# Performance work log

Measured on AMD Instinct MI355X. Metric: run time of the kernel, lower is better.

The kernel has to match this reference:

```python
import jax, jax.numpy as jnp
import numpy as np


def _retain(o1, others, W, bias):
    # o1: (b, s, h); others: (b, 4, s, h); W: (h, h); bias: (1,)
    q = o1 @ W                                        # (b, s, h)
    scores = jnp.einsum('bih,bkjh->bijk', q, others) + bias[0]  # (b, s1, s2, 4)
    w = jax.nn.softmax(scores, axis=-1)               # softmax over the 4 options
    # weight[:, :, :, k] @ option_k summed over k
    return jnp.einsum('bijk,bkjh->bih', w, others)


def setup_inputs() -> dict:
    key = jax.random.key(0)
    ks = jax.random.split(key, 7)
    b, s, h = 32, 256, 1024
    opts = {f'option{i+1}': jax.random.normal(ks[i], (b, s, h), dtype=jnp.float32)
            for i in range(5)}
    W = 0.02 * jax.random.normal(ks[5], (h, h), dtype=jnp.float32)
    bias = 0.02 * jax.random.normal(ks[6], (1,), dtype=jnp.float32)
    return {**opts, 'W': W, 'bias': bias}


def reference(option1, option2, option3, option4, option5, W, bias):
    opts = [option1, option2, option3, option4, option5]
    total = None
    for i in range(5):
        others = jnp.stack([opts[j] for j in range(5) if j != i], axis=1)  # (b,4,s,h)
        r = _retain(opts[i], others, W, bias)
        total = r if total is None else total + r
    return total / 2.0
```

## Files before the change

### kernel.cpp

```cpp
#include <hip/hip_runtime.h>
#include <hip/hip_bf16.h>
#include <stdint.h>


#define BB 32
#define SS 256
#define HH 1024

typedef __attribute__((ext_vector_type(4))) float f32x4;
typedef __attribute__((ext_vector_type(8))) __bf16 bf16x8;
typedef __attribute__((ext_vector_type(4))) __bf16 bf16x4;

__device__ constexpr int PAIR(int i, int n) { return i * 4 + (n > i ? n - 1 : n); }

__device__ __forceinline__ void gload_lds16(const void* g, void* l) {
  __builtin_amdgcn_global_load_lds((const __attribute__((address_space(1))) void*)g,
                                   (__attribute__((address_space(3))) void*)l, 16, 0, 0);
}

__global__ void canary(float* out, float v) { out[0] = v; }

__global__ __launch_bounds__(256) void cast_all(
    const float* p0, const float* p1, const float* p2, const float* p3, const float* p4,
    __bf16* __restrict__ dst)
{
  int m = blockIdx.x >> 12;
  long off = ((long)(blockIdx.x & 4095) * 256 + threadIdx.x) * 8;
  const float* src = m == 0 ? p0 : m == 1 ? p1 : m == 2 ? p2 : m == 3 ? p3 : p4;
  float4 v0 = *(const float4*)(src + off);
  float4 v1 = *(const float4*)(src + off + 4);
  bf16x8 h;
  h[0] = (__bf16)v0.x; h[1] = (__bf16)v0.y; h[2] = (__bf16)v0.z; h[3] = (__bf16)v0.w;
  h[4] = (__bf16)v1.x; h[5] = (__bf16)v1.y; h[6] = (__bf16)v1.z; h[7] = (__bf16)v1.w;
  *(bf16x8*)(dst + (long)m * BB * SS * HH + off) = h;
}

__global__ __launch_bounds__(256) void cast_trW(const float* __restrict__ src,
                                                __bf16* __restrict__ dstT)
{
  __shared__ __bf16 tile[64][72];
  int ct = blockIdx.x & 15, rt = blockIdx.x >> 4;
  const float* s = src + (long)(rt * 64) * 1024 + ct * 64;
  int t = threadIdx.x;
#pragma unroll
  for (int p = 0; p < 4; p++) {
    int c = t + p * 256;
    int row = c >> 4, c4 = c & 15;
    float4 v = *(const float4*)(s + (long)row * 1024 + c4 * 4);
    bf16x4 h;
    h[0] = (__bf16)v.x; h[1] = (__bf16)v.y; h[2] = (__bf16)v.z; h[3] = (__bf16)v.w;
    *(bf16x4*)&tile[row][c4 * 4] = h;
  }
  __syncthreads();
#pragma unroll
  for (int p = 0; p < 4; p++) {
    int c = t + p * 256;
    int hr = c >> 4, s4 = c & 15;
    bf16x4 h;
    h[0] = tile[s4 * 4 + 0][hr];
    h[1] = tile[s4 * 4 + 1][hr];
    h[2] = tile[s4 * 4 + 2][hr];
    h[3] = tile[s4 * 4 + 3][hr];
    *(bf16x4*)(dstT + (long)(ct * 64 + hr) * 1024 + rt * 64 + s4 * 4) = h;
  }
}

__global__ __launch_bounds__(256, 3) void qgemm_b16(
    const __bf16* __restrict__ A, const __bf16* __restrict__ Bt, __bf16* __restrict__ C)
{
  __shared__ __align__(16) char ldsb[3 * 16384];
  int lin = blockIdx.x;
  int xcd = lin & 7, idx = lin >> 3;
  int rt = xcd * 40 + (idx >> 3), ct = idx & 7;
  int t = threadIdx.x, l = t & 63, w = t >> 6;
  int wm = w >> 1, wn = w & 1;
  f32x4 acc[4][4] = {};

  const char *gA0, *gA1, *gB0, *gB1;
  {
    int c0 = t, c1 = t + 256;
    int r0 = c0 >> 2, h0 = (c0 & 3) ^ ((c0 >> 3) & 3);
    int r1 = c1 >> 2, h1 = (c1 & 3) ^ ((c1 >> 3) & 3);
    gA0 = (const char*)(A + (long)(rt * 128 + r0) * 1024 + h0 * 8);
    gA1 = (const char*)(A + (long)(rt * 128 + r1) * 1024 + h1 * 8);
    gB0 = (const char*)(Bt + (long)(ct * 128 + r0) * 1024 + h0 * 8);
    gB1 = (const char*)(Bt + (long)(ct * 128 + r1) * 1024 + h1 * 8);
  }
  int dst0 = w * 1024, dst1 = (w + 4) * 1024;

#define STAGE(BUF)                                                \
  {                                                               \
    char* base = ldsb + (BUF) * 16384;                            \
    gload_lds16(gA0, base + dst0); gA0 += 64;                     \
    gload_lds16(gA1, base + dst1); gA1 += 64;                     \
    gload_lds16(gB0, base + 8192 + dst0); gB0 += 64;              \
    gload_lds16(gB1, base + 8192 + dst1); gB1 += 64;              \
  }

  int lr = l & 15, sl = l >> 4;
  int swz = (sl ^ ((lr >> 1) & 3)) * 16;
  int aoff = (wm * 64 + lr) * 64 + swz;
  int boff = 8192 + (wn * 64 + lr) * 64 + swz;

#define COMPUTE(BUF)                                                                   \
  {                                                                                    \
    const char* base = ldsb + (BUF) * 16384;                                           \
    bf16x8 af[4], bfr[4];                                                              \
    _Pragma("unroll") for (int i = 0; i < 4; i++) {                                    \
      af[i]  = *(const bf16x8*)(base + aoff + i * 1024);                               \
      bfr[i] = *(const bf16x8*)(base + boff + i * 1024);                               \
    }                                                                                  \
    __builtin_amdgcn_s_setprio(1);                                                     \
    _Pragma("unroll") for (int i = 0; i < 4; i++)                                      \
      _Pragma("unroll") for (int j = 0; j < 4; j++)                                    \
        acc[i][j] = __builtin_amdgcn_mfma_f32_16x16x32_bf16(af[i], bfr[j],             \
                                                            acc[i][j], 0, 0, 0);       \
    __builtin_amdgcn_s_setprio(0);                                                     \
  }

#define STEP(CUR, STG)                                          \
  asm volatile("s_waitcnt vmcnt(4)" ::: "memory");              \
  __builtin_amdgcn_s_barrier();                                 \
  STAGE(STG);                                                   \
  COMPUTE(CUR);

  STAGE(0)
  STAGE(1)
  for (int it = 0; it < 10; it++) {
    STEP(0, 2)
    STEP(1, 0)
    STEP(2, 1)
  }
  asm volatile("s_waitcnt vmcnt(4)" ::: "memory");
  __builtin_amdgcn_s_barrier();
  COMPUTE(0)
  asm volatile("s_waitcnt vmcnt(0)" ::: "memory");
  __builtin_amdgcn_s_barrier();
  COMPUTE(1)
#undef STEP
#undef COMPUTE
#undef STAGE

#pragma unroll
  for (int i = 0; i < 4; i++) {
    long mrow = (long)rt * 128 + wm * 64 + i * 16 + ((l >> 4) << 2);
#pragma unroll
    for (int j = 0; j < 4; j++) {
      int n = ct * 128 + wn * 64 + j * 16 + (l & 15);
#pragma unroll
      for (int r = 0; r < 4; r++)
        C[(mrow + r) * 1024 + n] = (__bf16)acc[i][j][r];
    }
  }
}

__global__ __launch_bounds__(256, 2) void gram_b16(
    const __bf16* __restrict__ Q, const __bf16* __restrict__ O, __bf16* __restrict__ V)
{
  __shared__ __align__(16) char ldsb[3 * 20480];
  int bid = blockIdx.x;
  int xcd = bid & 7, idx = bid >> 3;
  int b = xcd * 4 + (idx >> 6);
  int rem = idx & 63;
  int s1t = rem >> 3, s2t = rem & 7;
  int t = threadIdx.x, l = t & 63, w = t >> 6;
  int pr = w >> 1, pc = w & 1;
  f32x4 acc[20] = {};

  long qrow0 = (long)b * SS + s1t * 32;
  long orow0 = (long)b * SS + s2t * 32;
  int slog = (l & 3) ^ ((l >> 3) & 3);
  const char* gp0; const char* gp1; const char* gp2; const char* gp3; const char* gp4;
#define GP_INIT(GP, P)                                                                \
  {                                                                                   \
    int g = 4 * (P) + w;                                                              \
    int isQ = g < 10;                                                                 \
    int gg = isQ ? g : g - 10;                                                        \
    long row = (long)(gg >> 1) * (BB * SS) + (isQ ? qrow0 : orow0) + (g & 1) * 16 +   \
               (l >> 2);                                                              \
    GP = (const char*)((isQ ? Q : O) + row * HH + slog * 8);                          \
  }
  GP_INIT(gp0, 0) GP_INIT(gp1, 1) GP_INIT(gp2, 2) GP_INIT(gp3, 3) GP_INIT(gp4, 4)
#undef GP_INIT
  int g0 = w, g1 = 4 + w, g2 = 8 + w, g3 = 12 + w, g4 = 16 + w;

#define STAGE(BB_)                                                      \
  {                                                                     \
    char* base = ldsb + (BB_) * 20480;                                  \
    gload_lds16(gp0, base + g0 * 1024); gp0 += 64;                      \
    gload_lds16(gp1, base + g1 * 1024); gp1 += 64;                      \
    gload_lds16(gp2, base + g2 * 1024); gp2 += 64;                      \
    gload_lds16(gp3, base + g3 * 1024); gp3 += 64;                      \
    gload_lds16(gp4, base + g4 * 1024); gp4 += 64;                      \
  }

  int lr = l & 15, sl = l >> 4;
  int swz = (sl ^ ((lr >> 1) & 3)) * 16;
  int qoff = (pr * 16 + lr) * 64 + swz;
  int ooff = 10240 + (pc * 16 + lr) * 64 + swz;

#define COMPUTE(BB_)                                                                   \
  {                                                                                    \
    const char* base = ldsb + (BB_) * 20480;                                           \
    bf16x8 qf[5], of[5];                                                               \
    _Pragma("unroll") for (int m = 0; m < 5; m++) {                                    \
      qf[m] = *(const bf16x8*)(base + m * 2048 + qoff);                                \
      of[m] = *(const bf16x8*)(base + m * 2048 + ooff);                                \
    }                                                                                  \
    __builtin_amdgcn_s_setprio(1);                                                     \
    _Pragma("unroll") for (int i = 0; i < 5; i++) {                                    \
      _Pragma("unroll") for (int n = 0; n < 5; n++) {                                  \
        if (n != i)                                                                    \
          acc[PAIR(i, n)] =                                                            \
              __builtin_amdgcn_mfma_f32_16x16x32_bf16(qf[i], of[n], acc[PAIR(i, n)],   \
                                                      0, 0, 0);                        \
      }                                                                                \
    }                                                                                  \
    __builtin_amdgcn_s_setprio(0);                                                     \
  }

#define STEP(CUR, STG)                                          \
  asm volatile("s_waitcnt vmcnt(5)" ::: "memory");              \
  __builtin_amdgcn_s_barrier();                                 \
  STAGE(STG);                                                   \
  COMPUTE(CUR);

  STAGE(0)
  STAGE(1)
  for (int it = 0; it < 10; it++) {
    STEP(0, 2)
    STEP(1, 0)
    STEP(2, 1)
  }
  asm volatile("s_waitcnt vmcnt(5)" ::: "memory");
  __builtin_amdgcn_s_barrier();
  COMPUTE(0)
  asm volatile("s_waitcnt vmcnt(0)" ::: "memory");
  __builtin_amdgcn_s_barrier();
  COMPUTE(1)
#undef STEP
#undef COMPUTE
#undef STAGE

  int s1g = s1t * 32 + pr * 16 + ((l >> 4) << 2);
  int s2g = s2t * 32 + pc * 16 + (l & 15);
#pragma unroll
  for (int r = 0; r < 4; r++) {
    float vacc[5] = {0.f, 0.f, 0.f, 0.f, 0.f};
#pragma unroll
    for (int i = 0; i < 5; i++) {
      float gg[5];
      float mx = -3.0e38f;
#pragma unroll
      for (int n = 0; n < 5; n++)
        if (n != i) { gg[n] = acc[PAIR(i, n)][r]; mx = fmaxf(mx, gg[n]); }
      float ee[5], ssum = 0.f;
#pragma unroll
      for (int n = 0; n < 5; n++)
        if (n != i) { ee[n] = __expf(gg[n] - mx); ssum += ee[n]; }
      float inv = 1.0f / ssum;
#pragma unroll
      for (int n = 0; n < 5; n++)
        if (n != i) vacc[n] += ee[n] * inv;
    }
#pragma unroll
    for (int n = 0; n < 5; n++)
      V[((long)(n * 32 + b) * 256 + s1g + r) * 256 + s2g] = (__bf16)vacc[n];
  }
}

__global__ __launch_bounds__(256) void pvgemm(
    const __bf16* __restrict__ Vb, const __bf16* __restrict__ Obf, float* __restrict__ out)
{
  __shared__ __bf16 smA[128][40];
  __shared__ __bf16 smB[128][40];
  int bid = blockIdx.x;
  int b = bid >> 4, s1t = (bid >> 3) & 1, ht = bid & 7;
  int t = threadIdx.x, l = t & 63, w = t >> 6;
  int wm = w >> 1, wn = w & 1;
  f32x4 acc[4][4] = {};
#pragma unroll
  for (int n = 0; n < 5; n++) {
    const __bf16* On = Obf + (long)n * BB * SS * HH;
    for (int st2 = 0; st2 < 8; st2++) {
      int s20 = st2 * 32;
#pragma unroll
      for (int p = 0; p < 2; p++) {
        int c = t + p * 256;
        int row = c >> 2, sl = c & 3;
        *(bf16x8*)&smA[row][sl * 8] =
            *(const bf16x8*)(Vb + (long)(n * BB + b) * SS * SS + (long)(s1t * 128 + row) * SS +
                             s20 + sl * 8);
      }
      {
        int h4 = (t & 31) * 4, s2q = (t >> 5) * 4;
        const __bf16* src = On + ((long)b * 256 + s20 + s2q) * 1024 + ht * 128 + h4;
        bf16x4 v0 = *(const bf16x4*)(src);
        bf16x4 v1 = *(const bf16x4*)(src + 1024);
        bf16x4 v2 = *(const bf16x4*)(src + 2048);
        bf16x4 v3 = *(const bf16x4*)(src + 3072);
        bf16x4 c0, c1, c2, c3;
        c0[0] = v0[0]; c0[1] = v1[0]; c0[2] = v2[0]; c0[3] = v3[0];
        c1[0] = v0[1]; c1[1] = v1[1]; c1[2] = v2[1]; c1[3] = v3[1];
        c2[0] = v0[2]; c2[1] = v1[2]; c2[2] = v2[2]; c2[3] = v3[2];
        c3[0] = v0[3]; c3[1] = v1[3]; c3[2] = v2[3]; c3[3] = v3[3];
        *(bf16x4*)&smB[h4 + 0][s2q] = c0;
        *(bf16x4*)&smB[h4 + 1][s2q] = c1;
        *(bf16x4*)&smB[h4 + 2][s2q] = c2;
        *(bf16x4*)&smB[h4 + 3][s2q] = c3;
      }
      __syncthreads();
      bf16x8 af[4], bfr[4];
      int sl = l >> 4, lr = l & 15;
#pragma unroll
      for (int i = 0; i < 4; i++) {
        af[i]  = *(const bf16x8*)&smA[wm * 64 + i * 16 + lr][sl * 8];
        bfr[i] = *(const bf16x8*)&smB[wn * 64 + i * 16 + lr][sl * 8];
      }
#pragma unroll
      for (int i = 0; i < 4; i++)
#pragma unroll
        for (int j = 0; j < 4; j++)
          acc[i][j] = __builtin_amdgcn_mfma_f32_16x16x32_bf16(af[i], bfr[j], acc[i][j], 0, 0, 0);
      __syncthreads();
    }
  }
#pragma unroll
  for (int i = 0; i < 4; i++) {
    int m = s1t * 128 + wm * 64 + i * 16 + ((l >> 4) << 2);
#pragma unroll
    for (int j = 0; j < 4; j++) {
      int n = ht * 128 + wn * 64 + j * 16 + (l & 15);
#pragma unroll
      for (int r = 0; r < 4; r++)
        out[(long)(b * SS + m + r) * HH + n] = 0.5f * acc[i][j][r];
    }
  }
}

extern "C" void kernel_launch(void* const* d_in, const int* in_sizes, int n_in,
                              void* d_out, int out_size, void* d_ws, size_t ws_size,
                              hipStream_t stream)
{
  const size_t SZ_W = (size_t)HH * HH * 2;
  const size_t SZ_Q = (size_t)5 * BB * SS * HH * 2;
  const size_t SZ_V = (size_t)5 * BB * SS * SS * 2;
  const size_t SZ_O = (size_t)5 * BB * SS * HH * 2;
  const size_t NEED = SZ_W + SZ_Q + SZ_V + SZ_O;
  if (ws_size < NEED) {
    canary<<<1, 1, 0, stream>>>((float*)d_out, (float)(ws_size >> 20));
    return;
  }
  char* ws = (char*)d_ws;
  __bf16* Wt  = (__bf16*)ws;
  __bf16* Qb  = (__bf16*)(ws + SZ_W);
  __bf16* Vb  = (__bf16*)(ws + SZ_W + SZ_Q);
  __bf16* Obf = (__bf16*)(ws + SZ_W + SZ_Q + SZ_V);
  const float* o0 = (const float*)d_in[0];
  const float* o1 = (const float*)d_in[1];
  const float* o2 = (const float*)d_in[2];
  const float* o3 = (const float*)d_in[3];
  const float* o4 = (const float*)d_in[4];

  cast_trW<<<256, 256, 0, stream>>>((const float*)d_in[5], Wt);
  cast_all<<<5 * 4096, 256, 0, stream>>>(o0, o1, o2, o3, o4, Obf);
  qgemm_b16<<<2560, 256, 0, stream>>>(Obf, Wt, Qb);
  gram_b16<<<2048, 256, 0, stream>>>(Qb, Obf, Vb);
  pvgemm<<<512, 256, 0, stream>>>(Vb, Obf, (float*)d_out);
}
```

Measured before the change: 294.9 us.

## Double-buffer LDS fragment reads in registers to overlap with MFMA

Restructures the K-loop so the LDS reads for the next k-step go into a second set of register fragments while the 20 MFMAs run on the current set. Global-to-LDS staging is primed three buffers deep before the loop starts. The loop is unrolled by two, and explicit lgkmcnt waits sit after each MFMA block. This is meant to hide LDS read latency behind matrix compute, at the cost of extra VGPRs for the second set of fragments and a longer epilogue.

```diff
diff --git a/kernel.cpp b/kernel.cpp
--- a/kernel.cpp
+++ b/kernel.cpp
@@ -184,9 +184,9 @@
 #undef GP_INIT
   int g0 = w, g1 = 4 + w, g2 = 8 + w, g3 = 12 + w, g4 = 16 + w;
 
-#define STAGE(BB_)                                                      \
+#define STAGE(BUF)                                                      \
   {                                                                     \
-    char* base = ldsb + (BB_) * 20480;                                  \
+    char* base = ldsb + (BUF) * 20480;                                  \
     gload_lds16(gp0, base + g0 * 1024); gp0 += 64;                      \
     gload_lds16(gp1, base + g1 * 1024); gp1 += 64;                      \
     gload_lds16(gp2, base + g2 * 1024); gp2 += 64;                      \
@@ -199,47 +199,80 @@
   int qoff = (pr * 16 + lr) * 64 + swz;
   int ooff = 10240 + (pc * 16 + lr) * 64 + swz;
 
-#define COMPUTE(BB_)                                                                   \
+  bf16x8 qE[5], oE[5], qO[5], oO[5];
+
+#define LOADF(QF, OF, BUF)                                                    \
+  {                                                                           \
+    const char* base = ldsb + (BUF) * 20480;                                  \
+    _Pragma("unroll") for (int m = 0; m < 5; m++) {                           \
+      QF[m] = *(const bf16x8*)(base + m * 2048 + qoff);                       \
+      OF[m] = *(const bf16x8*)(base + m * 2048 + ooff);                       \
+    }                                                                         \
+  }
+
+#define MFMA20(QF, OF)                                                                 \
   {                                                                                    \
-    const char* base = ldsb + (BB_) * 20480;                                           \
-    bf16x8 qf[5], of[5];                                                               \
-    _Pragma("unroll") for (int m = 0; m < 5; m++) {                                    \
-      qf[m] = *(const bf16x8*)(base + m * 2048 + qoff);                                \
-      of[m] = *(const bf16x8*)(base + m * 2048 + ooff);                                \
-    }                                                                                  \
     __builtin_amdgcn_s_setprio(1);                                                     \
     _Pragma("unroll") for (int i = 0; i < 5; i++) {                                    \
       _Pragma("unroll") for (int n = 0; n < 5; n++) {                                  \
         if (n != i)                                                                    \
           acc[PAIR(i, n)] =                                                            \
-              __builtin_amdgcn_mfma_f32_16x16x32_bf16(qf[i], of[n], acc[PAIR(i, n)],   \
+              __builtin_amdgcn_mfma_f32_16x16x32_bf16(QF[i], OF[n], acc[PAIR(i, n)],   \
                                                       0, 0, 0);                        \
       }                                                                                \
     }                                                                                  \
     __builtin_amdgcn_s_setprio(0);                                                     \
   }
 
-#define STEP(CUR, STG)                                          \
-  asm volatile("s_waitcnt vmcnt(5)" ::: "memory");              \
-  __builtin_amdgcn_s_barrier();                                 \
-  STAGE(STG);                                                   \
-  COMPUTE(CUR);
+#define VMC5  asm volatile("s_waitcnt vmcnt(5)" ::: "memory")
+#define VMC0  asm volatile("s_waitcnt vmcnt(0)" ::: "memory")
+#define LGK0  asm volatile("s_waitcnt lgkmcnt(0)" ::: "memory")
 
   STAGE(0)
   STAGE(1)
-  for (int it = 0; it < 10; it++) {
-    STEP(0, 2)
-    STEP(1, 0)
-    STEP(2, 1)
-  }
-  asm volatile("s_waitcnt vmcnt(5)" ::: "memory");
-  __builtin_amdgcn_s_barrier();
-  COMPUTE(0)
-  asm volatile("s_waitcnt vmcnt(0)" ::: "memory");
-  __builtin_amdgcn_s_barrier();
-  COMPUTE(1)
-#undef STEP
-#undef COMPUTE
+  STAGE(2)
+  asm volatile("s_waitcnt vmcnt(10)" ::: "memory");
+  __builtin_amdgcn_s_barrier();
+  LOADF(qE, oE, 0)
+  LGK0;
+
+  int bS = 0, bL = 1;
+  for (int it = 0; it < 14; it++) {
+    VMC5;
+    __builtin_amdgcn_s_barrier();
+    STAGE(bS); bS = bS == 2 ? 0 : bS + 1;
+    LOADF(qO, oO, bL) bL = bL == 2 ? 0 : bL + 1;
+    MFMA20(qE, oE)
+    LGK0;
+    VMC5;
+    __builtin_amdgcn_s_barrier();
+    STAGE(bS); bS = bS == 2 ? 0 : bS + 1;
+    LOADF(qE, oE, bL) bL = bL == 2 ? 0 : bL + 1;
+    MFMA20(qO, oO)
+    LGK0;
+  }
+  VMC5;
+  __builtin_amdgcn_s_barrier();
+  STAGE(bS);
+  LOADF(qO, oO, bL) bL = bL == 2 ? 0 : bL + 1;
+  MFMA20(qE, oE)
+  LGK0;
+  VMC5;
+  __builtin_amdgcn_s_barrier();
+  LOADF(qE, oE, bL) bL = bL == 2 ? 0 : bL + 1;
+  MFMA20(qO, oO)
+  LGK0;
+  VMC0;
+  __builtin_amdgcn_s_barrier();
+  LOADF(qO, oO, bL)
+  MFMA20(qE, oE)
+  LGK0;
+  MFMA20(qO, oO)
+#undef VMC5
+#undef VMC0
+#undef LGK0
+#undef MFMA20
+#undef LOADF
 #undef STAGE
 
   int s1g = s1t * 32 + pr * 16 + ((l >> 4) << 2);
```

Measured after the change: 293.0 us. No clear change (-0.6%).

## Load O fragments directly to registers and stage only Q through LDS

Applied to the files above, without the earlier changes.

The gram kernel no longer stages the O tiles through LDS. Each lane now reads its O MFMA fragments straight from global memory into registers, split into low and high halves that are prefetched one step ahead. Only Q goes through the triple-buffered LDS pipeline, now in 128-byte K-steps with two LOADQ/MFMA20 phases per stage. This cuts LDS traffic and bank pressure and raises the MFMA work done per barrier, but adds uncoalesced 16-byte global loads, higher register use, and a more complex vmcnt accounting.

```diff
diff --git a/kernel.cpp b/kernel.cpp
--- a/kernel.cpp
+++ b/kernel.cpp
@@ -170,77 +170,102 @@
   long qrow0 = (long)b * SS + s1t * 32;
   long orow0 = (long)b * SS + s2t * 32;
   int slog = (l & 3) ^ ((l >> 3) & 3);
-  const char* gp0; const char* gp1; const char* gp2; const char* gp3; const char* gp4;
-#define GP_INIT(GP, P)                                                                \
-  {                                                                                   \
-    int g = 4 * (P) + w;                                                              \
-    int isQ = g < 10;                                                                 \
-    int gg = isQ ? g : g - 10;                                                        \
-    long row = (long)(gg >> 1) * (BB * SS) + (isQ ? qrow0 : orow0) + (g & 1) * 16 +   \
-               (l >> 2);                                                              \
-    GP = (const char*)((isQ ? Q : O) + row * HH + slog * 8);                          \
-  }
-  GP_INIT(gp0, 0) GP_INIT(gp1, 1) GP_INIT(gp2, 2) GP_INIT(gp3, 3) GP_INIT(gp4, 4)
-#undef GP_INIT
-  int g0 = w, g1 = 4 + w, g2 = 8 + w, g3 = 12 + w, g4 = 16 + w;
-
-#define STAGE(BB_)                                                      \
+
+  const char* qp[5];
+  int qdst[5];
+#pragma unroll
+  for (int p = 0; p < 5; p++) {
+    long row = qrow0 + (long)p * (BB * SS) + (w >> 1) * 16 + (l >> 2);
+    qp[p] = (const char*)(Q + row * HH + (w & 1) * 32 + slog * 8);
+    qdst[p] = (w + 4 * p) * 1024;
+  }
+
+  int lr = l & 15, sl = l >> 4;
+  const char* op[5];
+#pragma unroll
+  for (int m = 0; m < 5; m++) {
+    long row = orow0 + (long)m * (BB * SS) + pc * 16 + lr;
+    op[m] = (const char*)(O + row * HH + sl * 8);
+  }
+
+  int swz = (sl ^ ((lr >> 1) & 3)) * 16;
+  int qsub = pr * 2;
+
+  bf16x8 qf[5], oLo[5], oHi[5];
+
+#define QSTAGE(BUF)                                                     \
   {                                                                     \
-    char* base = ldsb + (BB_) * 20480;                                  \
-    gload_lds16(gp0, base + g0 * 1024); gp0 += 64;                      \
-    gload_lds16(gp1, base + g1 * 1024); gp1 += 64;                      \
-    gload_lds16(gp2, base + g2 * 1024); gp2 += 64;                      \
-    gload_lds16(gp3, base + g3 * 1024); gp3 += 64;                      \
-    gload_lds16(gp4, base + g4 * 1024); gp4 += 64;                      \
-  }
-
-  int lr = l & 15, sl = l >> 4;
-  int swz = (sl ^ ((lr >> 1) & 3)) * 16;
-  int qoff = (pr * 16 + lr) * 64 + swz;
-  int ooff = 10240 + (pc * 16 + lr) * 64 + swz;
-
-#define COMPUTE(BB_)                                                                   \
+    char* base = ldsb + (BUF) * 20480;                                  \
+    _Pragma("unroll") for (int p = 0; p < 5; p++) {                     \
+      gload_lds16(qp[p], base + qdst[p]);                               \
+      qp[p] += 128;                                                     \
+    }                                                                   \
+  }
+
+#define LOADQ(BUF, H)                                                             \
+  {                                                                               \
+    const char* base = ldsb + (BUF) * 20480;                                      \
+    _Pragma("unroll") for (int m = 0; m < 5; m++)                                 \
+      qf[m] = *(const bf16x8*)(base + (m * 4 + qsub + (H)) * 1024 + lr * 64 + swz); \
+  }
+
+#define MFMA20(OF)                                                                     \
   {                                                                                    \
-    const char* base = ldsb + (BB_) * 20480;                                           \
-    bf16x8 qf[5], of[5];                                                               \
-    _Pragma("unroll") for (int m = 0; m < 5; m++) {                                    \
-      qf[m] = *(const bf16x8*)(base + m * 2048 + qoff);                                \
-      of[m] = *(const bf16x8*)(base + m * 2048 + ooff);                                \
-    }                                                                                  \
     __builtin_amdgcn_s_setprio(1);                                                     \
     _Pragma("unroll") for (int i = 0; i < 5; i++) {                                    \
       _Pragma("unroll") for (int n = 0; n < 5; n++) {                                  \
         if (n != i)                                                                    \
           acc[PAIR(i, n)] =                                                            \
-              __builtin_amdgcn_mfma_f32_16x16x32_bf16(qf[i], of[n], acc[PAIR(i, n)],   \
+              __builtin_amdgcn_mfma_f32_16x16x32_bf16(qf[i], OF[n], acc[PAIR(i, n)],   \
                                                       0, 0, 0);                        \
       }                                                                                \
     }                                                                                  \
     __builtin_amdgcn_s_setprio(0);                                                     \
   }
 
-#define STEP(CUR, STG)                                          \
-  asm volatile("s_waitcnt vmcnt(5)" ::: "memory");              \
-  __builtin_amdgcn_s_barrier();                                 \
-  STAGE(STG);                                                   \
-  COMPUTE(CUR);
-
-  STAGE(0)
-  STAGE(1)
-  for (int it = 0; it < 10; it++) {
-    STEP(0, 2)
-    STEP(1, 0)
-    STEP(2, 1)
-  }
-  asm volatile("s_waitcnt vmcnt(5)" ::: "memory");
-  __builtin_amdgcn_s_barrier();
-  COMPUTE(0)
-  asm volatile("s_waitcnt vmcnt(0)" ::: "memory");
-  __builtin_amdgcn_s_barrier();
-  COMPUTE(1)
-#undef STEP
-#undef COMPUTE
-#undef STAGE
+#define OHI_LOAD                                                         \
+  _Pragma("unroll") for (int m = 0; m < 5; m++)                          \
+      oHi[m] = *(const bf16x8*)(op[m] + 64);
+
+#define OLO_NEXT                                                         \
+  _Pragma("unroll") for (int m = 0; m < 5; m++) {                        \
+    op[m] += 128;                                                        \
+    oLo[m] = *(const bf16x8*)(op[m]);                                    \
+  }
+
+#define SUPER(CUR, STG, DOSTAGE, DOLO)                          \
+  {                                                             \
+    asm volatile("s_waitcnt vmcnt(10)" ::: "memory");           \
+    __builtin_amdgcn_s_barrier();                               \
+    OHI_LOAD                                                    \
+    if (DOSTAGE) { QSTAGE(STG) }                                \
+    LOADQ(CUR, 0)                                               \
+    MFMA20(oLo)                                                 \
+    if (DOLO) { OLO_NEXT }                                      \
+    LOADQ(CUR, 1)                                               \
+    MFMA20(oHi)                                                 \
+  }
+
+  QSTAGE(0)
+  QSTAGE(1)
+#pragma unroll
+  for (int m = 0; m < 5; m++) oLo[m] = *(const bf16x8*)(op[m]);
+
+  for (int it = 0; it < 4; it++) {
+    SUPER(0, 2, 1, 1)
+    SUPER(1, 0, 1, 1)
+    SUPER(2, 1, 1, 1)
+  }
+  SUPER(0, 2, 1, 1)
+  SUPER(1, 0, 1, 1)
+  SUPER(2, 0, 0, 1)
+  SUPER(0, 0, 0, 0)
+#undef SUPER
+#undef OLO_NEXT
+#undef OHI_LOAD
+#undef MFMA20
+#undef LOADQ
+#undef QSTAGE
 
   int s1g = s1t * 32 + pr * 16 + ((l >> 4) << 2);
   int s2g = s2t * 32 + pc * 16 + (l & 15);
```

Measured after the change: 357.5 us. +21.2%, slower.

## Retile gram kernel to 64x64 tiles with 32x32x16 MFMA

Applied to the files above, without the earlier changes.

The gram kernel now gives each block a 64x64 s1/s2 tile instead of 32x32, with each wave computing 32x32 per pair using the 32x32x16 bf16 MFMA. The staging layout and k-step (16 elements per stage, 64 stages) change to match, and the grid drops from 2048 to 512 blocks. The aim is to raise data reuse per loaded byte and cut LDS traffic per flop. In exchange, 20 accumulators of 16 floats each put heavy pressure on registers (launch bounds now allow one block per CU), and 512 blocks may leave parts of the machine underused. The new LDS layout drops the XOR swizzle, which may add bank conflicts.

```diff
diff --git a/kernel.cpp b/kernel.cpp
--- a/kernel.cpp
+++ b/kernel.cpp
@@ -8,6 +8,7 @@
 #define HH 1024
 
 typedef __attribute__((ext_vector_type(4))) float f32x4;
+typedef __attribute__((ext_vector_type(16))) float f32x16;
 typedef __attribute__((ext_vector_type(8))) __bf16 bf16x8;
 typedef __attribute__((ext_vector_type(4))) __bf16 bf16x4;
 
@@ -154,66 +155,57 @@
   }
 }
 
-__global__ __launch_bounds__(256, 2) void gram_b16(
+__global__ __launch_bounds__(256, 1) void gram32(
     const __bf16* __restrict__ Q, const __bf16* __restrict__ O, __bf16* __restrict__ V)
 {
   __shared__ __align__(16) char ldsb[3 * 20480];
   int bid = blockIdx.x;
   int xcd = bid & 7, idx = bid >> 3;
-  int b = xcd * 4 + (idx >> 6);
-  int rem = idx & 63;
-  int s1t = rem >> 3, s2t = rem & 7;
+  int b = xcd * 4 + (idx >> 4);
+  int rem = idx & 15;
+  int s1t = rem >> 2, s2t = rem & 3;
   int t = threadIdx.x, l = t & 63, w = t >> 6;
   int pr = w >> 1, pc = w & 1;
-  f32x4 acc[20] = {};
-
-  long qrow0 = (long)b * SS + s1t * 32;
-  long orow0 = (long)b * SS + s2t * 32;
-  int slog = (l & 3) ^ ((l >> 3) & 3);
-  const char* gp0; const char* gp1; const char* gp2; const char* gp3; const char* gp4;
-#define GP_INIT(GP, P)                                                                \
-  {                                                                                   \
-    int g = 4 * (P) + w;                                                              \
-    int isQ = g < 10;                                                                 \
-    int gg = isQ ? g : g - 10;                                                        \
-    long row = (long)(gg >> 1) * (BB * SS) + (isQ ? qrow0 : orow0) + (g & 1) * 16 +   \
-               (l >> 2);                                                              \
-    GP = (const char*)((isQ ? Q : O) + row * HH + slog * 8);                          \
-  }
-  GP_INIT(gp0, 0) GP_INIT(gp1, 1) GP_INIT(gp2, 2) GP_INIT(gp3, 3) GP_INIT(gp4, 4)
-#undef GP_INIT
-  int g0 = w, g1 = 4 + w, g2 = 8 + w, g3 = 12 + w, g4 = 16 + w;
-
-#define STAGE(BB_)                                                      \
+  f32x16 acc[20] = {};
+
+  const char* gp[5];
+  int udst[5];
+#pragma unroll
+  for (int p = 0; p < 5; p++) {
+    int c = t + 256 * p;
+    int mq = c >> 7, ch = (c >> 6) & 1, row = c & 63;
+    long grow = mq < 5 ? ((long)mq * (BB * SS) + (long)b * SS + s1t * 64 + row)
+                       : ((long)(mq - 5) * (BB * SS) + (long)b * SS + s2t * 64 + row);
+    gp[p] = (const char*)(mq < 5 ? Q : O) + grow * (HH * 2) + ch * 16;
+    udst[p] = ((t & ~63) + 256 * p) * 16;
+  }
+
+  int qro = (l >> 5) * 1024 + (pr * 32 + (l & 31)) * 16;
+  int oro = 10240 + (l >> 5) * 1024 + (pc * 32 + (l & 31)) * 16;
+
+#define QSTAGE(BUF)                                                     \
   {                                                                     \
-    char* base = ldsb + (BB_) * 20480;                                  \
-    gload_lds16(gp0, base + g0 * 1024); gp0 += 64;                      \
-    gload_lds16(gp1, base + g1 * 1024); gp1 += 64;                      \
-    gload_lds16(gp2, base + g2 * 1024); gp2 += 64;                      \
-    gload_lds16(gp3, base + g3 * 1024); gp3 += 64;                      \
-    gload_lds16(gp4, base + g4 * 1024); gp4 += 64;                      \
-  }
-
-  int lr = l & 15, sl = l >> 4;
-  int swz = (sl ^ ((lr >> 1) & 3)) * 16;
-  int qoff = (pr * 16 + lr) * 64 + swz;
-  int ooff = 10240 + (pc * 16 + lr) * 64 + swz;
-
-#define COMPUTE(BB_)                                                                   \
+    char* base = ldsb + (BUF) * 20480;                                  \
+    _Pragma("unroll") for (int p = 0; p < 5; p++) {                     \
+      gload_lds16(gp[p], base + udst[p]);                               \
+      gp[p] += 32;                                                      \
+    }                                                                   \
+  }
+
+#define MFMA_STEP(BUF)                                                                 \
   {                                                                                    \
-    const char* base = ldsb + (BB_) * 20480;                                           \
+    const char* base = ldsb + (BUF) * 20480;                                           \
     bf16x8 qf[5], of[5];                                                               \
     _Pragma("unroll") for (int m = 0; m < 5; m++) {                                    \
-      qf[m] = *(const bf16x8*)(base + m * 2048 + qoff);                                \
-      of[m] = *(const bf16x8*)(base + m * 2048 + ooff);                                \
+      qf[m] = *(const bf16x8*)(base + m * 2048 + qro);                                 \
+      of[m] = *(const bf16x8*)(base + m * 2048 + oro);                                 \
     }                                                                                  \
     __builtin_amdgcn_s_setprio(1);                                                     \
     _Pragma("unroll") for (int i = 0; i < 5; i++) {                                    \
       _Pragma("unroll") for (int n = 0; n < 5; n++) {                                  \
         if (n != i)                                                                    \
-          acc[PAIR(i, n)] =                                                            \
-              __builtin_amdgcn_mfma_f32_16x16x32_bf16(qf[i], of[n], acc[PAIR(i, n)],   \
-                                                      0, 0, 0);                        \
+          acc[PAIR(i, n)] = __builtin_amdgcn_mfma_f32_32x32x16_bf16(                   \
+              qf[i], of[n], acc[PAIR(i, n)], 0, 0, 0);                                 \
       }                                                                                \
     }                                                                                  \
     __builtin_amdgcn_s_setprio(0);                                                     \
@@ -222,30 +214,33 @@
 #define STEP(CUR, STG)                                          \
   asm volatile("s_waitcnt vmcnt(5)" ::: "memory");              \
   __builtin_amdgcn_s_barrier();                                 \
-  STAGE(STG);                                                   \
-  COMPUTE(CUR);
-
-  STAGE(0)
-  STAGE(1)
-  for (int it = 0; it < 10; it++) {
+  QSTAGE(STG);                                                  \
+  MFMA_STEP(CUR);
+
+  QSTAGE(0)
+  QSTAGE(1)
+  for (int it = 0; it < 20; it++) {
     STEP(0, 2)
     STEP(1, 0)
     STEP(2, 1)
   }
+  STEP(0, 2)
+  STEP(1, 0)
   asm volatile("s_waitcnt vmcnt(5)" ::: "memory");
   __builtin_amdgcn_s_barrier();
-  COMPUTE(0)
+  MFMA_STEP(2)
   asm volatile("s_waitcnt vmcnt(0)" ::: "memory");
   __builtin_amdgcn_s_barrier();
-  COMPUTE(1)
+  MFMA_STEP(0)
 #undef STEP
-#undef COMPUTE
-#undef STAGE
-
-  int s1g = s1t * 32 + pr * 16 + ((l >> 4) << 2);
-  int s2g = s2t * 32 + pc * 16 + (l & 15);
-#pragma unroll
-  for (int r = 0; r < 4; r++) {
+#undef MFMA_STEP
+#undef QSTAGE
+
+  int s2g = s2t * 64 + pc * 32 + (l & 31);
+  int s1b = s1t * 64 + pr * 32 + 4 * (l >> 5);
+#pragma unroll
+  for (int r = 0; r < 16; r++) {
+    int s1 = s1b + (r & 3) + 8 * (r >> 2);
     float vacc[5] = {0.f, 0.f, 0.f, 0.f, 0.f};
 #pragma unroll
     for (int i = 0; i < 5; i++) {
@@ -265,7 +260,7 @@
     }
 #pragma unroll
     for (int n = 0; n < 5; n++)
-      V[((long)(n * 32 + b) * 256 + s1g + r) * 256 + s2g] = (__bf16)vacc[n];
+      V[((long)(n * BB + b) * SS + s1) * SS + s2g] = (__bf16)vacc[n];
   }
 }
 
@@ -365,6 +360,6 @@
   cast_trW<<<256, 256, 0, stream>>>((const float*)d_in[5], Wt);
   cast_all<<<5 * 4096, 256, 0, stream>>>(o0, o1, o2, o3, o4, Obf);
   qgemm_b16<<<2560, 256, 0, stream>>>(Obf, Wt, Qb);
-  gram_b16<<<2048, 256, 0, stream>>>(Qb, Obf, Vb);
+  gram32<<<512, 256, 0, stream>>>(Qb, Obf, Vb);
   pvgemm<<<512, 256, 0, stream>>>(Vb, Obf, (float*)d_out);
 }
```

Result: slower. 381.4 us (+29.3%).
